# Optimization experiments

Hardware: AMD Instinct MI355X
Metric: run time of the kernel (lower is better)

## Reference

```python
import jax, jax.numpy as jnp
import numpy as np

B, N, K = 4, 4096, 16
D_POINTS, D_MODEL = 64, 128
SCALE = 1.0 / np.sqrt(float(D_MODEL))  # attn / sqrt(k.size(-1))


def _gather(points, idx):
    # points: [B, N, C], idx: [B, N, K] -> [B, N, K, C]  (index_points)
    return jax.vmap(lambda p, i: p[i])(points, idx)


def setup_inputs() -> dict:
    key = jax.random.key(0)
    ks = jax.random.split(key, 16)
    def w(k, shape, fan_in):
        return jax.random.normal(k, shape, jnp.float32) * (1.0 / np.sqrt(fan_in))
    return {
        "xyz": jax.random.normal(ks[0], (B, N, 3), jnp.float32),
        "features": jax.random.normal(ks[1], (B, N, D_POINTS), jnp.float32),
        "fc1_w": w(ks[2], (D_POINTS, D_MODEL), D_POINTS),
        "fc1_b": jnp.zeros((D_MODEL,), jnp.float32),
        "fc2_w": w(ks[3], (D_MODEL, D_POINTS), D_MODEL),
        "fc2_b": jnp.zeros((D_POINTS,), jnp.float32),
        "d1_w": w(ks[4], (3, D_MODEL), 3),
        "d1_b": jnp.zeros((D_MODEL,), jnp.float32),
        "d2_w": w(ks[5], (D_MODEL, D_MODEL), D_MODEL),
        "d2_b": jnp.zeros((D_MODEL,), jnp.float32),
        "g1_w": w(ks[6], (D_MODEL, D_MODEL), D_MODEL),
        "g1_b": jnp.zeros((D_MODEL,), jnp.float32),
        "g2_w": w(ks[7], (D_MODEL, D_MODEL), D_MODEL),
        "g2_b": jnp.zeros((D_MODEL,), jnp.float32),
        "wq_w": w(ks[8], (D_MODEL, D_MODEL), D_MODEL),
        "wk_w": w(ks[9], (D_MODEL, D_MODEL), D_MODEL),
        "wv_w": w(ks[10], (D_MODEL, D_MODEL), D_MODEL),
    }


def reference(xyz, features, fc1_w, fc1_b, fc2_w, fc2_b,
              d1_w, d1_b, d2_w, d2_b, g1_w, g1_b, g2_w, g2_b,
              wq_w, wk_w, wv_w):
    # knn_points(xyz, xyz, K): K nearest neighbors by squared distance
    d2 = jnp.sum((xyz[:, :, None, :] - xyz[:, None, :, :]) ** 2, axis=-1)  # [B,N,N]
    _, idx = jax.lax.top_k(-d2, K)                                         # [B,N,K]
    local_xyz = _gather(xyz, idx)                                          # [B,N,K,3]

    pre = features
    x = features @ fc1_w + fc1_b                                           # [B,N,dm]
    q = x @ wq_w                                                           # [B,N,dm]
    k_feat = _gather(x @ wk_w, idx)                                        # [B,N,K,dm]
    v = _gather(x @ wv_w, idx)                                             # [B,N,K,dm]

    # fc_delta(xyz[:, :, None] - local_xyz)
    rel = xyz[:, :, None, :] - local_xyz                                   # [B,N,K,3]
    pos_enc = jax.nn.relu(rel @ d1_w + d1_b) @ d2_w + d2_b                 # [B,N,K,dm]

    # fc_gamma(q[:, :, None] - k + pos_enc)
    h = q[:, :, None, :] - k_feat + pos_enc
    attn = jax.nn.relu(h @ g1_w + g1_b) @ g2_w + g2_b                      # [B,N,K,dm]
    attn = jax.nn.softmax(attn * SCALE, axis=-2)                           # softmax over K

    res = jnp.einsum('bmnf,bmnf->bmf', attn, v + pos_enc)                  # [B,N,dm]
    out = res @ fc2_w + fc2_b + pre                                        # [B,N,dp]
    return out, attn
```

## Files before the change

### kernel.cpp

```cpp
#include <hip/hip_runtime.h>

#define BATCH 4
#define NPTS  4096
#define KNN   16
#define DP    64
#define DM    128
#define PT_SCALE 0.08838834764831845f

typedef short bf16x8 __attribute__((ext_vector_type(8)));
typedef float f32x4 __attribute__((ext_vector_type(4)));

__device__ __forceinline__ unsigned short f2b(float f) {
  unsigned u = __float_as_uint(f);
  return (unsigned short)((u + 0x7FFFu + ((u >> 16) & 1u)) >> 16);
}
__device__ __forceinline__ float b2f(unsigned short u) {
  return __uint_as_float(((unsigned)u) << 16);
}

__global__ __launch_bounds__(256) void knn_kernel(const float* __restrict__ xyz,
                                                  int* __restrict__ idx_out) {
  const int wv = threadIdx.x >> 6, lane = threadIdx.x & 63;
  const int qid = blockIdx.x * 4 + wv;
  const int b = qid >> 12, n = qid & 4095;
  const float* xb = xyz + (size_t)b * NPTS * 3;
  const float qx = xb[n * 3 + 0], qy = xb[n * 3 + 1], qz = xb[n * 3 + 2];

  unsigned long long kk = 0xFFFFFFFFFFFFFFFFULL;
  for (int j0 = 0; j0 < NPTS; j0 += 64) {
    const int j = j0 + lane;
    const float cx = xb[j * 3 + 0], cy = xb[j * 3 + 1], cz = xb[j * 3 + 2];
    const float dx = __fsub_rn(qx, cx);
    const float dy = __fsub_rn(qy, cy);
    const float dz = __fsub_rn(qz, cz);
    const float d2 =
        __fadd_rn(__fadd_rn(__fmul_rn(dx, dx), __fmul_rn(dy, dy)), __fmul_rn(dz, dz));
    const unsigned long long key =
        ((unsigned long long)__float_as_uint(d2) << 32) | (unsigned int)j;
    const unsigned long long t = __shfl(kk, 15, 64);
    unsigned long long m = __ballot(key < t);
    while (m) {
      const int src = __ffsll((unsigned long long)m) - 1;
      m &= m - 1;
      const unsigned long long kv = __shfl(key, src, 64);
      const bool pr = kk > kv;
      const unsigned long long up = __shfl_up(kk, 1, 64);
      int pp = __shfl_up(pr ? 1 : 0, 1, 64);
      if (lane == 0) pp = 0;
      kk = pr ? (pp ? up : kv) : kk;
    }
  }
  if (lane < 16)
    idx_out[(size_t)qid * KNN + lane] = (int)(kk & 0xFFFFFFFFULL);
}

__global__ __launch_bounds__(256) void prep_kernel(const float* __restrict__ d2_w,
                                                   const float* __restrict__ g1_w,
                                                   const float* __restrict__ g2_w,
                                                   unsigned short* __restrict__ pk) {
  const float* W = blockIdx.x == 0 ? d2_w : (blockIdx.x == 1 ? g1_w : g2_w);
  unsigned short* o = pk + (size_t)blockIdx.x * 16384;
  for (int e = threadIdx.x; e < 16384; e += 256) {
    const int i = e & 7, l = (e >> 3) & 63, fr = e >> 9;
    const int nt = fr >> 2, ks = fr & 3;
    const int k = (l >> 4) * 8 + i + 32 * ks;
    const int c = nt * 16 + (l & 15);
    o[e] = f2b(W[k * DM + c]);
  }
}

__global__ __launch_bounds__(256) void qkv_kernel(
    const float* __restrict__ features,
    const float* __restrict__ fc1_w, const float* __restrict__ fc1_b,
    const float* __restrict__ wq, const float* __restrict__ wk, const float* __restrict__ wv,
    unsigned short* __restrict__ q_full, unsigned short* __restrict__ k_full,
    unsigned short* __restrict__ v_full) {
  __shared__ float feat_s[16][DP];
  __shared__ float x_s[16][DM];
  const size_t row0 = (size_t)blockIdx.x * 16;

  for (int i = threadIdx.x; i < 16 * DP; i += 256)
    feat_s[i >> 6][i & 63] = features[row0 * DP + i];
  __syncthreads();

  const int col = threadIdx.x & 127;
  const int rg  = (threadIdx.x >> 7) * 8;
  {
    float acc[8];
    const float bias = fc1_b[col];
#pragma unroll
    for (int r = 0; r < 8; ++r) acc[r] = bias;
    for (int k = 0; k < DP; ++k) {
      const float w = fc1_w[k * DM + col];
#pragma unroll
      for (int r = 0; r < 8; ++r) acc[r] = fmaf(feat_s[rg + r][k], w, acc[r]);
    }
#pragma unroll
    for (int r = 0; r < 8; ++r) x_s[rg + r][col] = acc[r];
  }
  __syncthreads();

  const float* Ws[3] = {wq, wk, wv};
  unsigned short* Os[3] = {q_full, k_full, v_full};
#pragma unroll
  for (int m = 0; m < 3; ++m) {
    const float* W = Ws[m];
    float acc[8];
#pragma unroll
    for (int r = 0; r < 8; ++r) acc[r] = 0.f;
    for (int k = 0; k < DM; ++k) {
      const float w = W[k * DM + col];
#pragma unroll
      for (int r = 0; r < 8; ++r) acc[r] = fmaf(x_s[rg + r][k], w, acc[r]);
    }
    unsigned short* O = Os[m] + row0 * DM;
#pragma unroll
    for (int r = 0; r < 8; ++r) O[(rg + r) * DM + col] = f2b(acc[r]);
  }
}

__global__ __launch_bounds__(512, 2) void fused_attn_kernel(
    const float* __restrict__ xyz, const int* __restrict__ idxg,
    const unsigned short* __restrict__ qf, const unsigned short* __restrict__ kf,
    const unsigned short* __restrict__ vf,
    const unsigned short* __restrict__ d2pk, const unsigned short* __restrict__ g1pk,
    const unsigned short* __restrict__ g2pk,
    const float* __restrict__ d1_w, const float* __restrict__ d1_b,
    const float* __restrict__ d2_b, const float* __restrict__ g1_b,
    const float* __restrict__ g2_b,
    float* __restrict__ attn_out, float* __restrict__ res_ws) {
  __shared__ unsigned short g1s[16384];
  __shared__ unsigned short g2s[16384];
  __shared__ float sc[8][16 * 132];
  __shared__ float d1s[3 * DM];
  __shared__ float d1bs[DM], d2bs[DM], g1bs[DM], g2bs[DM];

  for (int i = threadIdx.x; i < 2048; i += 512) {
    ((uint4*)g1s)[i] = ((const uint4*)g1pk)[i];
    ((uint4*)g2s)[i] = ((const uint4*)g2pk)[i];
  }
  if (threadIdx.x < 384) d1s[threadIdx.x] = d1_w[threadIdx.x];
  if (threadIdx.x < DM) {
    d1bs[threadIdx.x] = d1_b[threadIdx.x];
    d2bs[threadIdx.x] = d2_b[threadIdx.x];
    g1bs[threadIdx.x] = g1_b[threadIdx.x];
    g2bs[threadIdx.x] = g2_b[threadIdx.x];
  }
  __syncthreads();

  const int wv = threadIdx.x >> 6, lane = threadIdx.x & 63;
  const int g = lane >> 4, c15 = lane & 15;
  float* S = sc[wv];

  for (int qi = 0; qi < 8; ++qi) {
    const int qid = (blockIdx.x * 8 + wv) * 8 + qi;
    const int b = qid >> 12, n = qid & 4095;
    const size_t bN = (size_t)b * NPTS;

    const int myidx = idxg[(size_t)qid * KNN + c15];
    int srow[4];
#pragma unroll
    for (int i = 0; i < 4; ++i) srow[i] = __shfl(myidx, 4 * g + i, 64);

    unsigned short kred[8][4], qred[8];
#pragma unroll
    for (int i = 0; i < 4; ++i) {
      const unsigned short* kr = kf + (bN + srow[i]) * DM;
#pragma unroll
      for (int nt = 0; nt < 8; ++nt) kred[nt][i] = kr[nt * 16 + c15];
    }
    const unsigned short* qr = qf + (size_t)qid * DM;
#pragma unroll
    for (int nt = 0; nt < 8; ++nt) qred[nt] = qr[nt * 16 + c15];

    const float* xq = xyz + (bN + n) * 3;
    const float* xn = xyz + (bN + myidx) * 3;
    const float rx = xq[0] - xn[0], ry = xq[1] - xn[1], rz = xq[2] - xn[2];
    bf16x8 a[4];
#pragma unroll
    for (int ks = 0; ks < 4; ++ks) {
#pragma unroll
      for (int i = 0; i < 8; ++i) {
        const int cc = g * 8 + i + 32 * ks;
        float t = fmaf(rx, d1s[cc], fmaf(ry, d1s[DM + cc], fmaf(rz, d1s[2 * DM + cc], d1bs[cc])));
        a[ks][i] = (short)f2b(t > 0.f ? t : 0.f);
      }
    }
    f32x4 pos[8];
#pragma unroll
    for (int nt = 0; nt < 8; ++nt) {
      const float bb = d2bs[nt * 16 + c15];
      f32x4 acc = {bb, bb, bb, bb};
#pragma unroll
      for (int ks = 0; ks < 4; ++ks) {
        const bf16x8 bfr = *(const bf16x8*)(d2pk + (((nt * 4 + ks) * 64 + lane) << 3));
        acc = __builtin_amdgcn_mfma_f32_16x16x32_bf16(a[ks], bfr, acc, 0, 0, 0);
      }
      pos[nt] = acc;
    }
#pragma unroll
    for (int nt = 0; nt < 8; ++nt) {
      const float qv = b2f(qred[nt]);
#pragma unroll
      for (int i = 0; i < 4; ++i)
        S[(4 * g + i) * 132 + nt * 16 + c15] = qv - b2f(kred[nt][i]) + pos[nt][i];
    }
    unsigned short vred[8][4];
#pragma unroll
    for (int i = 0; i < 4; ++i) {
      const unsigned short* vr = vf + (bN + srow[i]) * DM;
#pragma unroll
      for (int nt = 0; nt < 8; ++nt) vred[nt][i] = vr[nt * 16 + c15];
    }
#pragma unroll
    for (int ks = 0; ks < 4; ++ks) {
      const float* p = &S[c15 * 132 + g * 8 + 32 * ks];
      const float4 lo = *(const float4*)p, hi = *(const float4*)(p + 4);
      a[ks][0] = (short)f2b(lo.x); a[ks][1] = (short)f2b(lo.y);
      a[ks][2] = (short)f2b(lo.z); a[ks][3] = (short)f2b(lo.w);
      a[ks][4] = (short)f2b(hi.x); a[ks][5] = (short)f2b(hi.y);
      a[ks][6] = (short)f2b(hi.z); a[ks][7] = (short)f2b(hi.w);
    }
#pragma unroll
    for (int nt = 0; nt < 8; ++nt) {
      const float bb = g1bs[nt * 16 + c15];
      f32x4 acc = {bb, bb, bb, bb};
#pragma unroll
      for (int ks = 0; ks < 4; ++ks) {
        const bf16x8 bfr = *(const bf16x8*)&g1s[((nt * 4 + ks) * 64 + lane) << 3];
        acc = __builtin_amdgcn_mfma_f32_16x16x32_bf16(a[ks], bfr, acc, 0, 0, 0);
      }
#pragma unroll
      for (int i = 0; i < 4; ++i)
        S[(4 * g + i) * 132 + nt * 16 + c15] = acc[i] > 0.f ? acc[i] : 0.f;
    }
#pragma unroll
    for (int ks = 0; ks < 4; ++ks) {
      const float* p = &S[c15 * 132 + g * 8 + 32 * ks];
      const float4 lo = *(const float4*)p, hi = *(const float4*)(p + 4);
      a[ks][0] = (short)f2b(lo.x); a[ks][1] = (short)f2b(lo.y);
      a[ks][2] = (short)f2b(lo.z); a[ks][3] = (short)f2b(lo.w);
      a[ks][4] = (short)f2b(hi.x); a[ks][5] = (short)f2b(hi.y);
      a[ks][6] = (short)f2b(hi.z); a[ks][7] = (short)f2b(hi.w);
    }
    f32x4 lg[8];
#pragma unroll
    for (int nt = 0; nt < 8; ++nt) {
      const float bb = g2bs[nt * 16 + c15];
      f32x4 acc = {bb, bb, bb, bb};
#pragma unroll
      for (int ks = 0; ks < 4; ++ks) {
        const bf16x8 bfr = *(const bf16x8*)&g2s[((nt * 4 + ks) * 64 + lane) << 3];
        acc = __builtin_amdgcn_mfma_f32_16x16x32_bf16(a[ks], bfr, acc, 0, 0, 0);
      }
      lg[nt] = acc;
    }
#pragma unroll
    for (int nt = 0; nt < 8; ++nt) {
      float s0 = lg[nt][0] * PT_SCALE, s1 = lg[nt][1] * PT_SCALE;
      float s2 = lg[nt][2] * PT_SCALE, s3 = lg[nt][3] * PT_SCALE;
      float mx = fmaxf(fmaxf(s0, s1), fmaxf(s2, s3));
      mx = fmaxf(mx, __shfl_xor(mx, 16, 64));
      mx = fmaxf(mx, __shfl_xor(mx, 32, 64));
      const float e0 = __expf(s0 - mx), e1 = __expf(s1 - mx);
      const float e2 = __expf(s2 - mx), e3 = __expf(s3 - mx);
      float sm = e0 + e1 + e2 + e3;
      sm += __shfl_xor(sm, 16, 64);
      sm += __shfl_xor(sm, 32, 64);
      const float inv = 1.f / sm;
      lg[nt][0] = e0 * inv; lg[nt][1] = e1 * inv;
      lg[nt][2] = e2 * inv; lg[nt][3] = e3 * inv;
    }
    float* ab = attn_out + (size_t)qid * (KNN * DM);
    float red[8];
#pragma unroll
    for (int nt = 0; nt < 8; ++nt) {
      float r4 = 0.f;
#pragma unroll
      for (int i = 0; i < 4; ++i) {
        const float pp = lg[nt][i];
        ab[(4 * g + i) * DM + nt * 16 + c15] = pp;
        r4 = fmaf(pp, b2f(vred[nt][i]) + pos[nt][i], r4);
      }
      r4 += __shfl_xor(r4, 16, 64);
      r4 += __shfl_xor(r4, 32, 64);
      red[nt] = r4;
    }
    if (g == 0) {
      float* rw = res_ws + (size_t)qid * DM;
#pragma unroll
      for (int nt = 0; nt < 8; ++nt) rw[nt * 16 + c15] = red[nt];
    }
  }
}

__global__ __launch_bounds__(256) void out_kernel(
    const float* __restrict__ res, const float* __restrict__ fc2_w,
    const float* __restrict__ fc2_b, const float* __restrict__ feat,
    float* __restrict__ out) {
  __shared__ float rs[16][DM];
  const size_t row0 = (size_t)blockIdx.x * 16;
  for (int i = threadIdx.x; i < 16 * DM; i += 256)
    rs[i >> 7][i & 127] = res[row0 * DM + i];
  __syncthreads();
  const int col = threadIdx.x & 63;
  const int rg  = (threadIdx.x >> 6) * 4;
  float acc[4];
  const float bb = fc2_b[col];
#pragma unroll
  for (int r = 0; r < 4; ++r) acc[r] = bb + feat[(row0 + rg + r) * DP + col];
  for (int k = 0; k < DM; ++k) {
    const float w = fc2_w[k * DP + col];
#pragma unroll
    for (int r = 0; r < 4; ++r) acc[r] = fmaf(rs[rg + r][k], w, acc[r]);
  }
#pragma unroll
  for (int r = 0; r < 4; ++r) out[(row0 + rg + r) * DP + col] = acc[r];
}

extern "C" void kernel_launch(void* const* d_in, const int* in_sizes, int n_in,
                              void* d_out, int out_size, void* d_ws, size_t ws_size,
                              hipStream_t stream) {
  (void)in_sizes; (void)n_in; (void)out_size; (void)ws_size;
  const float* xyz      = (const float*)d_in[0];
  const float* features = (const float*)d_in[1];
  const float* fc1_w = (const float*)d_in[2];
  const float* fc1_b = (const float*)d_in[3];
  const float* fc2_w = (const float*)d_in[4];
  const float* fc2_b = (const float*)d_in[5];
  const float* d1_w  = (const float*)d_in[6];
  const float* d1_b  = (const float*)d_in[7];
  const float* d2_w  = (const float*)d_in[8];
  const float* d2_b  = (const float*)d_in[9];
  const float* g1_w  = (const float*)d_in[10];
  const float* g1_b  = (const float*)d_in[11];
  const float* g2_w  = (const float*)d_in[12];
  const float* g2_b  = (const float*)d_in[13];
  const float* wq_w  = (const float*)d_in[14];
  const float* wk_w  = (const float*)d_in[15];
  const float* wv_w  = (const float*)d_in[16];

  float* out  = (float*)d_out;
  float* attn = out + (size_t)BATCH * NPTS * DP;

  char* ws = (char*)d_ws;
  int*            idx_ws = (int*)ws;
  unsigned short* q_full = (unsigned short*)(ws + (1u << 20));
  unsigned short* k_full = (unsigned short*)(ws + (5u << 20));
  unsigned short* v_full = (unsigned short*)(ws + (9u << 20));
  float*          res_ws = (float*)(ws + (13u << 20));
  unsigned short* pk     = (unsigned short*)(ws + (21u << 20));

  prep_kernel<<<dim3(3), 256, 0, stream>>>(d2_w, g1_w, g2_w, pk);
  knn_kernel<<<dim3(4096), 256, 0, stream>>>(xyz, idx_ws);
  qkv_kernel<<<dim3(1024), 256, 0, stream>>>(features, fc1_w, fc1_b,
                                             wq_w, wk_w, wv_w,
                                             q_full, k_full, v_full);
  fused_attn_kernel<<<dim3(256), 512, 0, stream>>>(
      xyz, idx_ws, q_full, k_full, v_full, pk, pk + 16384, pk + 32768,
      d1_w, d1_b, d2_b, g1_b, g2_b, attn, res_ws);
  out_kernel<<<dim3(1024), 256, 0, stream>>>(res_ws, fc2_w, fc2_b, features, out);
}
```

Baseline: 497.9 us.

## Rework KNN to per-lane sorted lists with threshold pruning; shrink attention LDS

The KNN kernel now keeps a 16-entry sorted list in registers per lane and skips inserts unless some lane beats a wave-wide threshold. That threshold is refreshed every four iterations, and the lists are merged across lanes at the end. This replaces the serial ballot/shuffle insertion loop. The attention kernel stores its intermediate tiles as bf16 instead of fp32, reads g2 weights from global instead of LDS, and halves queries per wave so it can launch twice the blocks at three blocks per CU. The trade-offs are higher KNN register pressure and global reads of g2 weights in the inner MFMA loop.

```diff
diff --git a/kernel.cpp b/kernel.cpp
--- a/kernel.cpp
+++ b/kernel.cpp
@@ -5,6 +5,7 @@
 #define KNN   16
 #define DP    64
 #define DM    128
+#define SLD   136
 #define PT_SCALE 0.08838834764831845f
 
 typedef short bf16x8 __attribute__((ext_vector_type(8)));
@@ -26,32 +27,59 @@
   const float* xb = xyz + (size_t)b * NPTS * 3;
   const float qx = xb[n * 3 + 0], qy = xb[n * 3 + 1], qz = xb[n * 3 + 2];
 
-  unsigned long long kk = 0xFFFFFFFFFFFFFFFFULL;
-  for (int j0 = 0; j0 < NPTS; j0 += 64) {
-    const int j = j0 + lane;
+  unsigned long long kk[16];
+#pragma unroll
+  for (int s = 0; s < 16; ++s) kk[s] = 0xFFFFFFFFFFFFFFFFULL;
+  unsigned tau = 0xFFFFFFFFu;
+
+  for (int i = 0; i < 64; ++i) {
+    const int j = i * 64 + lane;
     const float cx = xb[j * 3 + 0], cy = xb[j * 3 + 1], cz = xb[j * 3 + 2];
     const float dx = __fsub_rn(qx, cx);
     const float dy = __fsub_rn(qy, cy);
     const float dz = __fsub_rn(qz, cz);
     const float d2 =
         __fadd_rn(__fadd_rn(__fmul_rn(dx, dx), __fmul_rn(dy, dy)), __fmul_rn(dz, dz));
-    const unsigned long long key =
-        ((unsigned long long)__float_as_uint(d2) << 32) | (unsigned int)j;
-    const unsigned long long t = __shfl(kk, 15, 64);
-    unsigned long long m = __ballot(key < t);
-    while (m) {
-      const int src = __ffsll((unsigned long long)m) - 1;
-      m &= m - 1;
-      const unsigned long long kv = __shfl(key, src, 64);
-      const bool pr = kk > kv;
-      const unsigned long long up = __shfl_up(kk, 1, 64);
-      int pp = __shfl_up(pr ? 1 : 0, 1, 64);
-      if (lane == 0) pp = 0;
-      kk = pr ? (pp ? up : kv) : kk;
+    const unsigned d2u = __float_as_uint(d2);
+    if (__any(d2u <= tau)) {
+      const unsigned long long key = ((unsigned long long)d2u << 32) | (unsigned int)j;
+      bool lt[16];
+#pragma unroll
+      for (int s = 0; s < 16; ++s) lt[s] = key < kk[s];
+#pragma unroll
+      for (int s = 15; s >= 1; --s) kk[s] = lt[s] ? (lt[s - 1] ? kk[s - 1] : key) : kk[s];
+      kk[0] = lt[0] ? key : kk[0];
+    }
+    if ((i & 3) == 3) {
+      unsigned t = (unsigned)(kk[15] >> 32);
+#pragma unroll
+      for (int d = 32; d >= 1; d >>= 1) {
+        const unsigned o = __shfl_xor(t, d, 64);
+        t = o < t ? o : t;
+      }
+      tau = t;
+    }
+  }
+
+  unsigned long long head = kk[0];
+  unsigned long long res = 0;
+  for (int r = 0; r < 16; ++r) {
+    unsigned long long m = head;
+#pragma unroll
+    for (int d = 32; d >= 1; d >>= 1) {
+      const unsigned long long o = __shfl_xor(m, d, 64);
+      m = o < m ? o : m;
+    }
+    if (lane == r) res = m;
+    if (head == m) {
+#pragma unroll
+      for (int s = 0; s < 15; ++s) kk[s] = kk[s + 1];
+      kk[15] = 0xFFFFFFFFFFFFFFFFULL;
+      head = kk[0];
     }
   }
   if (lane < 16)
-    idx_out[(size_t)qid * KNN + lane] = (int)(kk & 0xFFFFFFFFULL);
+    idx_out[(size_t)qid * KNN + lane] = (int)(res & 0xFFFFFFFFULL);
 }
 
 __global__ __launch_bounds__(256) void prep_kernel(const float* __restrict__ d2_w,
@@ -119,7 +147,7 @@
   }
 }
 
-__global__ __launch_bounds__(512, 2) void fused_attn_kernel(
+__global__ __launch_bounds__(512, 3) void fused_attn_kernel(
     const float* __restrict__ xyz, const int* __restrict__ idxg,
     const unsigned short* __restrict__ qf, const unsigned short* __restrict__ kf,
     const unsigned short* __restrict__ vf,
@@ -130,15 +158,12 @@
     const float* __restrict__ g2_b,
     float* __restrict__ attn_out, float* __restrict__ res_ws) {
   __shared__ unsigned short g1s[16384];
-  __shared__ unsigned short g2s[16384];
-  __shared__ float sc[8][16 * 132];
+  __shared__ unsigned short sc[8][16 * SLD];
   __shared__ float d1s[3 * DM];
   __shared__ float d1bs[DM], d2bs[DM], g1bs[DM], g2bs[DM];
 
-  for (int i = threadIdx.x; i < 2048; i += 512) {
+  for (int i = threadIdx.x; i < 2048; i += 512)
     ((uint4*)g1s)[i] = ((const uint4*)g1pk)[i];
-    ((uint4*)g2s)[i] = ((const uint4*)g2pk)[i];
-  }
   if (threadIdx.x < 384) d1s[threadIdx.x] = d1_w[threadIdx.x];
   if (threadIdx.x < DM) {
     d1bs[threadIdx.x] = d1_b[threadIdx.x];
@@ -150,10 +175,10 @@
 
   const int wv = threadIdx.x >> 6, lane = threadIdx.x & 63;
   const int g = lane >> 4, c15 = lane & 15;
-  float* S = sc[wv];
-
-  for (int qi = 0; qi < 8; ++qi) {
-    const int qid = (blockIdx.x * 8 + wv) * 8 + qi;
+  unsigned short* S = sc[wv];
+
+  for (int qi = 0; qi < 4; ++qi) {
+    const int qid = (blockIdx.x * 8 + wv) * 4 + qi;
     const int b = qid >> 12, n = qid & 4095;
     const size_t bN = (size_t)b * NPTS;
 
@@ -162,13 +187,7 @@
 #pragma unroll
     for (int i = 0; i < 4; ++i) srow[i] = __shfl(myidx, 4 * g + i, 64);
 
-    unsigned short kred[8][4], qred[8];
-#pragma unroll
-    for (int i = 0; i < 4; ++i) {
-      const unsigned short* kr = kf + (bN + srow[i]) * DM;
-#pragma unroll
-      for (int nt = 0; nt < 8; ++nt) kred[nt][i] = kr[nt * 16 + c15];
-    }
+    unsigned short qred[8];
     const unsigned short* qr = qf + (size_t)qid * DM;
 #pragma unroll
     for (int nt = 0; nt < 8; ++nt) qred[nt] = qr[nt * 16 + c15];
@@ -199,11 +218,13 @@
       pos[nt] = acc;
     }
 #pragma unroll
-    for (int nt = 0; nt < 8; ++nt) {
-      const float qv = b2f(qred[nt]);
-#pragma unroll
-      for (int i = 0; i < 4; ++i)
-        S[(4 * g + i) * 132 + nt * 16 + c15] = qv - b2f(kred[nt][i]) + pos[nt][i];
+    for (int i = 0; i < 4; ++i) {
+      const unsigned short* kr = kf + (bN + srow[i]) * DM;
+#pragma unroll
+      for (int nt = 0; nt < 8; ++nt) {
+        const float hv = b2f(qred[nt]) - b2f(kr[nt * 16 + c15]) + pos[nt][i];
+        S[(4 * g + i) * SLD + nt * 16 + c15] = f2b(hv);
+      }
     }
     unsigned short vred[8][4];
 #pragma unroll
@@ -213,14 +234,8 @@
       for (int nt = 0; nt < 8; ++nt) vred[nt][i] = vr[nt * 16 + c15];
     }
 #pragma unroll
-    for (int ks = 0; ks < 4; ++ks) {
-      const float* p = &S[c15 * 132 + g * 8 + 32 * ks];
-      const float4 lo = *(const float4*)p, hi = *(const float4*)(p + 4);
-      a[ks][0] = (short)f2b(lo.x); a[ks][1] = (short)f2b(lo.y);
-      a[ks][2] = (short)f2b(lo.z); a[ks][3] = (short)f2b(lo.w);
-      a[ks][4] = (short)f2b(hi.x); a[ks][5] = (short)f2b(hi.y);
-      a[ks][6] = (short)f2b(hi.z); a[ks][7] = (short)f2b(hi.w);
-    }
+    for (int ks = 0; ks < 4; ++ks)
+      a[ks] = *(const bf16x8*)&S[c15 * SLD + g * 8 + 32 * ks];
 #pragma unroll
     for (int nt = 0; nt < 8; ++nt) {
       const float bb = g1bs[nt * 16 + c15];
@@ -232,17 +247,11 @@
       }
 #pragma unroll
       for (int i = 0; i < 4; ++i)
-        S[(4 * g + i) * 132 + nt * 16 + c15] = acc[i] > 0.f ? acc[i] : 0.f;
-    }
-#pragma unroll
-    for (int ks = 0; ks < 4; ++ks) {
-      const float* p = &S[c15 * 132 + g * 8 + 32 * ks];
-      const float4 lo = *(const float4*)p, hi = *(const float4*)(p + 4);
-      a[ks][0] = (short)f2b(lo.x); a[ks][1] = (short)f2b(lo.y);
-      a[ks][2] = (short)f2b(lo.z); a[ks][3] = (short)f2b(lo.w);
-      a[ks][4] = (short)f2b(hi.x); a[ks][5] = (short)f2b(hi.y);
-      a[ks][6] = (short)f2b(hi.z); a[ks][7] = (short)f2b(hi.w);
-    }
+        S[(4 * g + i) * SLD + nt * 16 + c15] = f2b(acc[i] > 0.f ? acc[i] : 0.f);
+    }
+#pragma unroll
+    for (int ks = 0; ks < 4; ++ks)
+      a[ks] = *(const bf16x8*)&S[c15 * SLD + g * 8 + 32 * ks];
     f32x4 lg[8];
 #pragma unroll
     for (int nt = 0; nt < 8; ++nt) {
@@ -250,7 +259,7 @@
       f32x4 acc = {bb, bb, bb, bb};
 #pragma unroll
       for (int ks = 0; ks < 4; ++ks) {
-        const bf16x8 bfr = *(const bf16x8*)&g2s[((nt * 4 + ks) * 64 + lane) << 3];
+        const bf16x8 bfr = *(const bf16x8*)(g2pk + (((nt * 4 + ks) * 64 + lane) << 3));
         acc = __builtin_amdgcn_mfma_f32_16x16x32_bf16(a[ks], bfr, acc, 0, 0, 0);
       }
       lg[nt] = acc;
@@ -356,7 +365,7 @@
   qkv_kernel<<<dim3(1024), 256, 0, stream>>>(features, fc1_w, fc1_b,
                                              wq_w, wk_w, wv_w,
                                              q_full, k_full, v_full);
-  fused_attn_kernel<<<dim3(256), 512, 0, stream>>>(
+  fused_attn_kernel<<<dim3(512), 512, 0, stream>>>(
       xyz, idx_ws, q_full, k_full, v_full, pk, pk + 16384, pk + 32768,
       d1_w, d1_b, d2_b, g1_b, g2_b, attn, res_ws);
   out_kernel<<<dim3(1024), 256, 0, stream>>>(res_ws, fc2_w, fc2_b, features, out);
```

Measured after the change: 714.6 us. 43.5% more time.
